# Performance work log

Measured on AMD Instinct MI355X. Metric: run time of the kernel, lower is better.

Reference implementation:

```python
import jax, jax.numpy as jnp
import numpy as np

N_NODES = 100000
N_EDGES = 640000
D_IN = 128
D_OUT = 128


def setup_inputs() -> dict:
    key = jax.random.key(0)
    k1, k2, k3, k4, k5 = jax.random.split(key, 5)
    feats = jax.random.normal(k1, (N_NODES, D_IN), dtype=jnp.float32)
    src = jax.random.randint(k2, (N_EDGES,), 0, N_NODES, dtype=jnp.int32)
    dst = jax.random.randint(k3, (N_EDGES,), 0, N_NODES, dtype=jnp.int32)
    # Xavier-normal-ish init (gain for relu = sqrt(2))
    std = float(np.sqrt(2.0) * np.sqrt(2.0 / (D_IN + D_OUT)))
    linear_skip_weight = jax.random.normal(k4, (D_OUT, D_IN), dtype=jnp.float32) * std
    linear_msg_weight = jax.random.normal(k5, (D_OUT, D_IN), dtype=jnp.float32) * std
    linear_skip_bias = jnp.zeros((D_OUT,), dtype=jnp.float32)
    linear_msg_bias = jnp.zeros((D_OUT,), dtype=jnp.float32)
    return {
        "feats": feats,
        "src": src,
        "dst": dst,
        "linear_skip_weight": linear_skip_weight,
        "linear_skip_bias": linear_skip_bias,
        "linear_msg_weight": linear_msg_weight,
        "linear_msg_bias": linear_msg_bias,
    }


def reference(feats, src, dst, linear_skip_weight, linear_skip_bias,
              linear_msg_weight, linear_msg_bias):
    n = feats.shape[0]
    # degree from scatter-add of edge weights (ones) at source rows
    deg = jax.ops.segment_sum(jnp.ones_like(src, dtype=feats.dtype), src,
                              num_segments=n)
    deg_inv_sqrt = jnp.where(deg > 0, jax.lax.rsqrt(jnp.maximum(deg, 1.0)) * (deg > 0), 0.0)
    deg_inv_sqrt = jnp.where(deg > 0, deg ** -0.5, 0.0)
    # normalize source features, gather along edges, scatter-sum to dst
    feat_src = feats * deg_inv_sqrt[:, None]           # [N, D_IN]
    msgs = feat_src[src]                               # [E, D_IN]
    rst = jax.ops.segment_sum(msgs, dst, num_segments=n)  # [N, D_IN]
    rst = rst * deg_inv_sqrt[:, None]
    rst_ = rst @ linear_msg_weight.T + linear_msg_bias
    skip_x = feats @ linear_skip_weight.T + linear_skip_bias
    return rst_ + skip_x
```

## Files before the change

### kernel.cpp

```cpp
#include <hip/hip_runtime.h>

#define N_NODES 100000
#define N_EDGES 640000
#define D 128
#define NB ((N_NODES + 1023) / 1024)

typedef short v8s __attribute__((ext_vector_type(8)));
typedef float v4f __attribute__((ext_vector_type(4)));

__device__ __forceinline__ unsigned short f2bf(float x) {
    unsigned int u = __builtin_bit_cast(unsigned int, x);
    u += 0x7fffu + ((u >> 16) & 1u);
    return (unsigned short)(u >> 16);
}
__device__ __forceinline__ float bf2f(unsigned int hi) {
    return __builtin_bit_cast(float, hi << 16);
}

__global__ __launch_bounds__(256) void k_pre(const float* __restrict__ feats,
                                             const float* __restrict__ Wm,
                                             const float* __restrict__ Ws,
                                             const float* __restrict__ bmsg,
                                             const float* __restrict__ bskip,
                                             int* __restrict__ z,
                                             unsigned short* __restrict__ Bcat,
                                             float* __restrict__ bias,
                                             char* __restrict__ outb) {
    int i = blockIdx.x * blockDim.x + threadIdx.x;
    if (i < 3 * N_NODES) z[i] = 0;
    if (i < D * D) {
        int j = i >> 7;
        int k = i & 127;
        Bcat[j * 256 + k]       = f2bf(Wm[i]);
        Bcat[j * 256 + 128 + k] = f2bf(Ws[i]);
    }
    if (i < D) bias[i] = bmsg[i] + bskip[i];
    int g = i * 8;
    int row = g >> 7;
    int col = g & 127;
    if (row < N_NODES) {
        const float4* s = (const float4*)(feats + g);
        float4 x = s[0], y = s[1];
        uint4 p;
        p.x = (unsigned)f2bf(x.x) | ((unsigned)f2bf(x.y) << 16);
        p.y = (unsigned)f2bf(x.z) | ((unsigned)f2bf(x.w) << 16);
        p.z = (unsigned)f2bf(y.x) | ((unsigned)f2bf(y.y) << 16);
        p.w = (unsigned)f2bf(y.z) | ((unsigned)f2bf(y.w) << 16);
        *(uint4*)(outb + (size_t)row * 512 + 256 + col * 2) = p;
    }
}

__global__ __launch_bounds__(256) void k_count(const int* __restrict__ src,
                                               const int* __restrict__ dst,
                                               int* __restrict__ deg_src,
                                               int* __restrict__ cnt_dst) {
    int e = blockIdx.x * blockDim.x + threadIdx.x;
    if (e < N_EDGES) {
        atomicAdd(&deg_src[src[e]], 1);
        atomicAdd(&cnt_dst[dst[e]], 1);
    }
}

__global__ __launch_bounds__(256) void k_scan1(const int* __restrict__ cnt,
                                               int* __restrict__ rowptr,
                                               int* __restrict__ bsums) {
    __shared__ int sd[256];
    int t = threadIdx.x;
    int i0 = blockIdx.x * 1024 + t * 4;
    int v[4];
    int s = 0;
#pragma unroll
    for (int q = 0; q < 4; q++) {
        int i = i0 + q;
        v[q] = (i < N_NODES) ? cnt[i] : 0;
        s += v[q];
    }
    sd[t] = s;
    __syncthreads();
    for (int off = 1; off < 256; off <<= 1) {
        int y = (t >= off) ? sd[t - off] : 0;
        __syncthreads();
        sd[t] += y;
        __syncthreads();
    }
    int run = sd[t] - s;
    if (t == 255) bsums[blockIdx.x] = sd[255];
#pragma unroll
    for (int q = 0; q < 4; q++) {
        int i = i0 + q;
        if (i < N_NODES) rowptr[i] = run;
        run += v[q];
    }
}

__global__ __launch_bounds__(128) void k_scan2(int* __restrict__ bsums,
                                               int* __restrict__ rowptr) {
    __shared__ int sd[128];
    int t = threadIdx.x;
    int v = (t < NB) ? bsums[t] : 0;
    sd[t] = v;
    __syncthreads();
    for (int off = 1; off < 128; off <<= 1) {
        int y = (t >= off) ? sd[t - off] : 0;
        __syncthreads();
        sd[t] += y;
        __syncthreads();
    }
    if (t < NB) bsums[t] = sd[t] - v;
    if (t == 0) rowptr[N_NODES] = N_EDGES;
}

__global__ __launch_bounds__(256) void k_scan3(const int* __restrict__ bsums,
                                               int* __restrict__ rowptr,
                                               const int* __restrict__ deg,
                                               float* __restrict__ dis) {
    int add = bsums[blockIdx.x];
    int i0 = blockIdx.x * 1024 + threadIdx.x * 4;
#pragma unroll
    for (int q = 0; q < 4; q++) {
        int i = i0 + q;
        if (i < N_NODES) {
            rowptr[i] += add;
            int d = deg[i];
            dis[i] = (d > 0) ? (1.0f / sqrtf((float)d)) : 0.0f;
        }
    }
}

__global__ __launch_bounds__(256) void k_fill(const int* __restrict__ src,
                                              const int* __restrict__ dst,
                                              const int* __restrict__ rowptr,
                                              int* __restrict__ cur,
                                              int* __restrict__ csr_src) {
    int e = blockIdx.x * blockDim.x + threadIdx.x;
    if (e < N_EDGES) {
        int d = dst[e];
        int p = atomicAdd(&cur[d], 1);
        csr_src[rowptr[d] + p] = src[e];
    }
}

__global__ __launch_bounds__(256) void k_agg(char* __restrict__ outb,
                                             const int* __restrict__ rowptr,
                                             const int* __restrict__ csr_src,
                                             const float* __restrict__ dis) {
    int wid = (int)((blockIdx.x * (unsigned)blockDim.x + threadIdx.x) >> 6);
    int lane = threadIdx.x & 63;
    if (wid >= N_NODES) return;
    int grp = lane >> 4;
    int sub = lane & 15;
    int start = rowptr[wid];
    int end = rowptr[wid + 1];
    float acc[8];
#pragma unroll
    for (int i = 0; i < 8; i++) acc[i] = 0.f;

    for (int base = start; base < end; base += 4) {
        int e = base + grp;
        if (e < end) {
            int s = csr_src[e];
            float sc = dis[s];
            uint4 v = *(const uint4*)(outb + (size_t)s * 512 + 256 + sub * 16);
            acc[0] += bf2f(v.x & 0xffffu) * sc;
            acc[1] += bf2f(v.x >> 16) * sc;
            acc[2] += bf2f(v.y & 0xffffu) * sc;
            acc[3] += bf2f(v.y >> 16) * sc;
            acc[4] += bf2f(v.z & 0xffffu) * sc;
            acc[5] += bf2f(v.z >> 16) * sc;
            acc[6] += bf2f(v.w & 0xffffu) * sc;
            acc[7] += bf2f(v.w >> 16) * sc;
        }
    }
#pragma unroll
    for (int i = 0; i < 8; i++) {
        acc[i] += __shfl_xor(acc[i], 16);
        acc[i] += __shfl_xor(acc[i], 32);
    }
    if (grp == 0) {
        float scn = dis[wid];
        uint4 p;
        p.x = (unsigned)f2bf(acc[0] * scn) | ((unsigned)f2bf(acc[1] * scn) << 16);
        p.y = (unsigned)f2bf(acc[2] * scn) | ((unsigned)f2bf(acc[3] * scn) << 16);
        p.z = (unsigned)f2bf(acc[4] * scn) | ((unsigned)f2bf(acc[5] * scn) << 16);
        p.w = (unsigned)f2bf(acc[6] * scn) | ((unsigned)f2bf(acc[7] * scn) << 16);
        *(uint4*)(outb + (size_t)wid * 512 + sub * 16) = p;
    }
}

__global__ __launch_bounds__(256) void k_gemm(const unsigned short* __restrict__ Bcat,
                                              const float* __restrict__ bias,
                                              float* __restrict__ outf) {
    __shared__ unsigned short Bl[128][264];
    const char* Ab = (const char*)outf;
    int tid = threadIdx.x;
    int lane = tid & 63;
    int w = tid >> 6;
    int n0 = blockIdx.x * 128;

    for (int i = tid; i < 128 * 32; i += 256) {
        int r = i >> 5, c = i & 31;
        *(uint4*)(&Bl[r][c * 8]) = *(const uint4*)(Bcat + r * 256 + c * 8);
    }
    __syncthreads();

    int q = lane >> 4;
    int lr = lane & 15;

    int r0 = n0 + w * 32 + lr;      if (r0 > N_NODES - 1) r0 = N_NODES - 1;
    int r1 = n0 + w * 32 + 16 + lr; if (r1 > N_NODES - 1) r1 = N_NODES - 1;
    const char* a0p = Ab + (size_t)r0 * 512 + q * 16;
    const char* a1p = Ab + (size_t)r1 * 512 + q * 16;

    v4f acc[2][8];
#pragma unroll
    for (int mt = 0; mt < 2; mt++)
#pragma unroll
        for (int t = 0; t < 8; t++) acc[mt][t] = (v4f){0.f, 0.f, 0.f, 0.f};

#pragma unroll
    for (int kk = 0; kk < 8; kk++) {
        v8s a0 = *(const v8s*)(a0p + kk * 64);
        v8s a1 = *(const v8s*)(a1p + kk * 64);
#pragma unroll
        for (int t = 0; t < 8; t++) {
            v8s b = *(const v8s*)(&Bl[t * 16 + lr][kk * 32 + q * 8]);
            acc[0][t] = __builtin_amdgcn_mfma_f32_16x16x32_bf16(a0, b, acc[0][t], 0, 0, 0);
            acc[1][t] = __builtin_amdgcn_mfma_f32_16x16x32_bf16(a1, b, acc[1][t], 0, 0, 0);
        }
    }

#pragma unroll
    for (int t = 0; t < 8; t++) {
        float bv = bias[t * 16 + lr];
#pragma unroll
        for (int mt = 0; mt < 2; mt++) {
            int rowb = n0 + w * 32 + mt * 16 + q * 4;
#pragma unroll
            for (int r = 0; r < 4; r++) {
                int row = rowb + r;
                if (row < N_NODES)
                    outf[(size_t)row * 128 + t * 16 + lr] = acc[mt][t][r] + bv;
            }
        }
    }
}

extern "C" void kernel_launch(void* const* d_in, const int* in_sizes, int n_in,
                              void* d_out, int out_size, void* d_ws, size_t ws_size,
                              hipStream_t stream) {
    const float* feats = (const float*)d_in[0];
    const int*   src   = (const int*)d_in[1];
    const int*   dst   = (const int*)d_in[2];
    const float* Wskip = (const float*)d_in[3];
    const float* bskip = (const float*)d_in[4];
    const float* Wmsg  = (const float*)d_in[5];
    const float* bmsg  = (const float*)d_in[6];

    char* w = (char*)d_ws;
    int*            deg_src = (int*)w;
    int*            cnt_dst = (int*)(w + 400000);
    int*            cur     = (int*)(w + 800000);
    float*          dis     = (float*)(w + 1200000);
    int*            rowptr  = (int*)(w + 1600000);
    int*            bsums   = (int*)(w + 2000128);
    unsigned short* Bcat    = (unsigned short*)(w + 2000640);
    float*          bias    = (float*)(w + 2066176);
    int*            csr_src = (int*)(w + 2066688);

    hipLaunchKernelGGL(k_pre, dim3((N_NODES * (D / 8) + 255) / 256), dim3(256), 0,
                       stream, feats, Wmsg, Wskip, bmsg, bskip, deg_src, Bcat, bias,
                       (char*)d_out);
    hipLaunchKernelGGL(k_count, dim3((N_EDGES + 255) / 256), dim3(256), 0, stream,
                       src, dst, deg_src, cnt_dst);
    hipLaunchKernelGGL(k_scan1, dim3(NB), dim3(256), 0, stream,
                       cnt_dst, rowptr, bsums);
    hipLaunchKernelGGL(k_scan2, dim3(1), dim3(128), 0, stream, bsums, rowptr);
    hipLaunchKernelGGL(k_scan3, dim3(NB), dim3(256), 0, stream, bsums, rowptr,
                       deg_src, dis);
    hipLaunchKernelGGL(k_fill, dim3((N_EDGES + 255) / 256), dim3(256), 0, stream,
                       src, dst, rowptr, cur, csr_src);
    hipLaunchKernelGGL(k_agg, dim3((N_NODES * 64 + 255) / 256), dim3(256), 0, stream,
                       (char*)d_out, rowptr, csr_src, dis);
    hipLaunchKernelGGL(k_gemm, dim3((N_NODES + 127) / 128), dim3(256), 0, stream,
                       Bcat, bias, (float*)d_out);
}
```

Baseline: 274.5 us.

## Pack src/dst degree counters into one word and fold counting into prep kernel

Packs the source-degree count (low 16 bits) and destination count (high 16 bits) into a single 32-bit word per node, so the two atomics hit the same array. The counting moves into k_pre, which removes the separate k_count launch. k_fill now bumps rowptr in place and gets the CSR slot directly, which drops the cur array and leaves each node's end offset in rowptr[i], so k_agg reads start from rowptr[i-1]. This cuts launches, workspace zeroing and memory traffic, but a node with 65536 or more edges on one side would overflow its 16-bit field, and k_zero adds a small launch of its own.

```diff
diff --git a/kernel.cpp b/kernel.cpp
--- a/kernel.cpp
+++ b/kernel.cpp
@@ -15,6 +15,11 @@
 }
 __device__ __forceinline__ float bf2f(unsigned int hi) {
     return __builtin_bit_cast(float, hi << 16);
+}
+
+__global__ __launch_bounds__(256) void k_zero(int4* __restrict__ pk4) {
+    int i = blockIdx.x * blockDim.x + threadIdx.x;
+    if (i < N_NODES / 4) pk4[i] = make_int4(0, 0, 0, 0);
 }
 
 __global__ __launch_bounds__(256) void k_pre(const float* __restrict__ feats,
@@ -22,12 +27,13 @@
                                              const float* __restrict__ Ws,
                                              const float* __restrict__ bmsg,
                                              const float* __restrict__ bskip,
-                                             int* __restrict__ z,
+                                             const int* __restrict__ src,
+                                             const int* __restrict__ dst,
+                                             unsigned int* __restrict__ pk,
                                              unsigned short* __restrict__ Bcat,
                                              float* __restrict__ bias,
                                              char* __restrict__ outb) {
     int i = blockIdx.x * blockDim.x + threadIdx.x;
-    if (i < 3 * N_NODES) z[i] = 0;
     if (i < D * D) {
         int j = i >> 7;
         int k = i & 127;
@@ -35,6 +41,10 @@
         Bcat[j * 256 + 128 + k] = f2bf(Ws[i]);
     }
     if (i < D) bias[i] = bmsg[i] + bskip[i];
+    if (i < N_EDGES) {
+        atomicAdd(&pk[src[i]], 1u);
+        atomicAdd(&pk[dst[i]], 0x10000u);
+    }
     int g = i * 8;
     int row = g >> 7;
     int col = g & 127;
@@ -50,18 +60,7 @@
     }
 }
 
-__global__ __launch_bounds__(256) void k_count(const int* __restrict__ src,
-                                               const int* __restrict__ dst,
-                                               int* __restrict__ deg_src,
-                                               int* __restrict__ cnt_dst) {
-    int e = blockIdx.x * blockDim.x + threadIdx.x;
-    if (e < N_EDGES) {
-        atomicAdd(&deg_src[src[e]], 1);
-        atomicAdd(&cnt_dst[dst[e]], 1);
-    }
-}
-
-__global__ __launch_bounds__(256) void k_scan1(const int* __restrict__ cnt,
+__global__ __launch_bounds__(256) void k_scan1(const unsigned int* __restrict__ pk,
                                                int* __restrict__ rowptr,
                                                int* __restrict__ bsums) {
     __shared__ int sd[256];
@@ -72,7 +71,7 @@
 #pragma unroll
     for (int q = 0; q < 4; q++) {
         int i = i0 + q;
-        v[q] = (i < N_NODES) ? cnt[i] : 0;
+        v[q] = (i < N_NODES) ? (int)(pk[i] >> 16) : 0;
         s += v[q];
     }
     sd[t] = s;
@@ -93,8 +92,7 @@
     }
 }
 
-__global__ __launch_bounds__(128) void k_scan2(int* __restrict__ bsums,
-                                               int* __restrict__ rowptr) {
+__global__ __launch_bounds__(128) void k_scan2(int* __restrict__ bsums) {
     __shared__ int sd[128];
     int t = threadIdx.x;
     int v = (t < NB) ? bsums[t] : 0;
@@ -107,12 +105,11 @@
         __syncthreads();
     }
     if (t < NB) bsums[t] = sd[t] - v;
-    if (t == 0) rowptr[N_NODES] = N_EDGES;
 }
 
 __global__ __launch_bounds__(256) void k_scan3(const int* __restrict__ bsums,
                                                int* __restrict__ rowptr,
-                                               const int* __restrict__ deg,
+                                               const unsigned int* __restrict__ pk,
                                                float* __restrict__ dis) {
     int add = bsums[blockIdx.x];
     int i0 = blockIdx.x * 1024 + threadIdx.x * 4;
@@ -121,7 +118,7 @@
         int i = i0 + q;
         if (i < N_NODES) {
             rowptr[i] += add;
-            int d = deg[i];
+            int d = (int)(pk[i] & 0xffffu);
             dis[i] = (d > 0) ? (1.0f / sqrtf((float)d)) : 0.0f;
         }
     }
@@ -129,14 +126,12 @@
 
 __global__ __launch_bounds__(256) void k_fill(const int* __restrict__ src,
                                               const int* __restrict__ dst,
-                                              const int* __restrict__ rowptr,
-                                              int* __restrict__ cur,
+                                              int* __restrict__ rowptr,
                                               int* __restrict__ csr_src) {
     int e = blockIdx.x * blockDim.x + threadIdx.x;
     if (e < N_EDGES) {
-        int d = dst[e];
-        int p = atomicAdd(&cur[d], 1);
-        csr_src[rowptr[d] + p] = src[e];
+        int p = atomicAdd(&rowptr[dst[e]], 1);
+        csr_src[p] = src[e];
     }
 }
 
@@ -149,8 +144,8 @@
     if (wid >= N_NODES) return;
     int grp = lane >> 4;
     int sub = lane & 15;
-    int start = rowptr[wid];
-    int end = rowptr[wid + 1];
+    int start = (wid == 0) ? 0 : rowptr[wid - 1];
+    int end = rowptr[wid];
     float acc[8];
 #pragma unroll
     for (int i = 0; i < 8; i++) acc[i] = 0.f;
@@ -257,28 +252,25 @@
     const float* bmsg  = (const float*)d_in[6];
 
     char* w = (char*)d_ws;
-    int*            deg_src = (int*)w;
-    int*            cnt_dst = (int*)(w + 400000);
-    int*            cur     = (int*)(w + 800000);
-    float*          dis     = (float*)(w + 1200000);
-    int*            rowptr  = (int*)(w + 1600000);
-    int*            bsums   = (int*)(w + 2000128);
-    unsigned short* Bcat    = (unsigned short*)(w + 2000640);
-    float*          bias    = (float*)(w + 2066176);
-    int*            csr_src = (int*)(w + 2066688);
-
+    unsigned int*   pk      = (unsigned int*)w;
+    float*          dis     = (float*)(w + 400000);
+    int*            rowptr  = (int*)(w + 800000);
+    int*            bsums   = (int*)(w + 1200128);
+    unsigned short* Bcat    = (unsigned short*)(w + 1200640);
+    float*          bias    = (float*)(w + 1266176);
+    int*            csr_src = (int*)(w + 1266688);
+
+    hipLaunchKernelGGL(k_zero, dim3((N_NODES / 4 + 255) / 256), dim3(256), 0, stream,
+                       (int4*)pk);
     hipLaunchKernelGGL(k_pre, dim3((N_NODES * (D / 8) + 255) / 256), dim3(256), 0,
-                       stream, feats, Wmsg, Wskip, bmsg, bskip, deg_src, Bcat, bias,
-                       (char*)d_out);
-    hipLaunchKernelGGL(k_count, dim3((N_EDGES + 255) / 256), dim3(256), 0, stream,
-                       src, dst, deg_src, cnt_dst);
-    hipLaunchKernelGGL(k_scan1, dim3(NB), dim3(256), 0, stream,
-                       cnt_dst, rowptr, bsums);
-    hipLaunchKernelGGL(k_scan2, dim3(1), dim3(128), 0, stream, bsums, rowptr);
+                       stream, feats, Wmsg, Wskip, bmsg, bskip, src, dst, pk, Bcat,
+                       bias, (char*)d_out);
+    hipLaunchKernelGGL(k_scan1, dim3(NB), dim3(256), 0, stream, pk, rowptr, bsums);
+    hipLaunchKernelGGL(k_scan2, dim3(1), dim3(128), 0, stream, bsums);
     hipLaunchKernelGGL(k_scan3, dim3(NB), dim3(256), 0, stream, bsums, rowptr,
-                       deg_src, dis);
+                       pk, dis);
     hipLaunchKernelGGL(k_fill, dim3((N_EDGES + 255) / 256), dim3(256), 0, stream,
-                       src, dst, rowptr, cur, csr_src);
+                       src, dst, rowptr, csr_src);
     hipLaunchKernelGGL(k_agg, dim3((N_NODES * 64 + 255) / 256), dim3(256), 0, stream,
                        (char*)d_out, rowptr, csr_src, dis);
     hipLaunchKernelGGL(k_gemm, dim3((N_NODES + 127) / 128), dim3(256), 0, stream,
```

After: 277.4 us. Within noise of the previous version (+1.1%).
